# Optimization experiments

Measured on AMD Instinct MI355X. Metric: run time of the kernel, lower is better.

## Reference

```python
import jax, jax.numpy as jnp
import numpy as np

VOCAB_SIZE = 119547  # bert-base-multilingual-cased
B, S, H = 64, 512, 768


def setup_inputs() -> dict:
    key = jax.random.key(0)
    k1, k2, k3, k4 = jax.random.split(key, 4)
    hidden_states = jax.random.normal(k1, (B, S, H), dtype=jnp.float32)
    input_ids = jax.random.randint(k2, (B, S), 0, VOCAB_SIZE, dtype=jnp.int64)
    attention_mask = jnp.ones((B, S), dtype=jnp.int32)
    W1 = jax.random.normal(k3, (H, H), dtype=jnp.float32) * (1.0 / np.sqrt(H))
    b1 = jnp.zeros((H,), dtype=jnp.float32)
    W2 = jax.random.normal(k4, (H, 1), dtype=jnp.float32) * (1.0 / np.sqrt(H))
    b2 = jnp.zeros((1,), dtype=jnp.float32)
    return {"hidden_states": hidden_states, "input_ids": input_ids,
            "attention_mask": attention_mask, "W1": W1, "b1": b1, "W2": W2, "b2": b2}


def reference(hidden_states, input_ids, attention_mask, W1, b1, W2, b2):
    # token_importance MLP (dropout = identity at eval): [B,S,H] -> [B,S]
    h = jax.nn.relu(jnp.einsum('bsh,hk->bsk', hidden_states, W1) + b1)
    importance = (jnp.einsum('bsh,ho->bso', h, W2) + b2)[..., 0]  # [B,S]
    token_weights = jnp.log1p(jax.nn.relu(importance)) * attention_mask.astype(jnp.float32)
    # scatter-max into vocab-sized sparse doc vector.
    # Masked positions have weight 0; buffer init 0 and weights >= 0, so
    # scattering 0 is equivalent to skipping them (matches the torch loop).
    batch_idx = jnp.arange(hidden_states.shape[0])[:, None]  # [B,1]
    sparse_repr = jnp.zeros((hidden_states.shape[0], VOCAB_SIZE), dtype=token_weights.dtype)
    sparse_repr = sparse_repr.at[batch_idx, input_ids].max(token_weights)
    return sparse_repr, token_weights
```

## Files before the change

kernel.cpp:

```cpp
#include <hip/hip_runtime.h>
#include <math.h>
#include <stdint.h>

#define VOCAB 119547
#define NB    64
#define NS    512
#define NH    768
#define M_TOT (NB * NS)

typedef _Float16 half8_t __attribute__((ext_vector_type(8)));
typedef _Float16 half4_t __attribute__((ext_vector_type(4)));
typedef float f32x4 __attribute__((ext_vector_type(4)));

__device__ __forceinline__ void gload_lds16(const void* g, void* l) {
    __builtin_amdgcn_global_load_lds(
        (const __attribute__((address_space(1))) uint32_t*)g,
        (__attribute__((address_space(3))) uint32_t*)l, 16, 0, 0);
}

__global__ void prep(const float* __restrict__ W1,
                     float4* __restrict__ sparse4, float* __restrict__ imp_,
                     _Float16* __restrict__ W1T) {
    long i = (long)blockIdx.x * blockDim.x + threadIdx.x;
    long stride = (long)gridDim.x * blockDim.x;
    const float4 z = make_float4(0.f, 0.f, 0.f, 0.f);
    const long nsp4 = (long)NB * VOCAB / 4;
    for (long j = i; j < nsp4; j += stride) sparse4[j] = z;
    float4* imp4 = (float4*)imp_;
    for (long j = i; j < M_TOT / 4; j += stride) imp4[j] = z;
    const long nw4 = (long)NH * NH / 4;
    half4_t* W1T4 = (half4_t*)W1T;
    for (long j = i; j < nw4; j += stride) {
        int n  = (int)(j / (NH / 4));
        int k4 = (int)(j % (NH / 4)) * 4;
        half4_t h;
#pragma unroll
        for (int q = 0; q < 4; ++q) h[q] = (_Float16)W1[(long)(k4 + q) * NH + n];
        W1T4[j] = h;
    }
}

__global__ __launch_bounds__(256, 4) void gemm_f16(
    const float* __restrict__ X,
    const _Float16* __restrict__ W1T,
    const float* __restrict__ b1,
    const float* __restrict__ W2v,
    float* __restrict__ imp)
{
    __shared__ __align__(16) _Float16 As[2][128 * 32];
    __shared__ __align__(16) _Float16 Bs[2][128 * 32];

    const int tid  = threadIdx.x;
    const int lane = tid & 63;
    const int wid  = tid >> 6;
    const int wm   = wid >> 1;
    const int wn   = wid & 1;

    const int bid = blockIdx.x;
    const int wg  = (bid & 7) * 192 + (bid >> 3);
    const int nt  = wg % 6;
    const int mt  = wg / 6;
    const int m0  = mt * 128;
    const int n0  = nt * 128;

    const int c0 = tid, c1 = tid + 256;
    const int r0 = c0 >> 2, r1 = c1 >> 2;
    const int sk0 = ((c0 & 3) ^ ((r0 >> 1) & 3)) * 8;
    const int sk1 = ((c1 & 3) ^ ((r1 >> 1) & 3)) * 8;
    const _Float16* gB0 = W1T + (long)(n0 + r0) * NH + sk0;
    const _Float16* gB1 = W1T + (long)(n0 + r1) * NH + sk1;

    const int ar = tid >> 3;
    const int kc = tid & 7;
    const float* gA = X + (long)(m0 + ar) * NH + kc * 4;
    const int aw = ((kc >> 1) ^ ((ar >> 1) & 3)) * 8 + (kc & 1) * 4;

    const int lr = lane & 15;
    const int ls = lane >> 4;
    const int s2 = ls ^ ((lr >> 1) & 3);
    int offA[4], offB[4];
#pragma unroll
    for (int f = 0; f < 4; ++f) {
        offA[f] = (wm * 64 + f * 16 + lr) * 32 + s2 * 8;
        offB[f] = (wn * 64 + f * 16 + lr) * 32 + s2 * 8;
    }

    f32x4 acc[4][4];
#pragma unroll
    for (int a = 0; a < 4; ++a)
#pragma unroll
        for (int b = 0; b < 4; ++b) acc[a][b] = (f32x4){0.f, 0.f, 0.f, 0.f};

    float4 Areg[4];

#define LOADA(T)                                                            \
    _Pragma("unroll") for (int i = 0; i < 4; ++i)                           \
        Areg[i] = *(const float4*)(gA + (T) * 32 + (long)i * 32 * NH);

#define CVTWRITE(BUF)                                                       \
    _Pragma("unroll") for (int i = 0; i < 4; ++i) {                         \
        half4_t h;                                                          \
        h[0] = (_Float16)Areg[i].x; h[1] = (_Float16)Areg[i].y;             \
        h[2] = (_Float16)Areg[i].z; h[3] = (_Float16)Areg[i].w;             \
        *(half4_t*)(As[BUF] + (ar + 32 * i) * 32 + aw) = h;                 \
    }

#define STAGEB(T, BUF)                                                      \
    gload_lds16(gB0 + (T) * 32, Bs[BUF] + c0 * 8);                          \
    gload_lds16(gB1 + (T) * 32, Bs[BUF] + c1 * 8);

#define COMPUTE(BUF)                                                        \
    {                                                                       \
        half8_t af[4], bf[4];                                               \
        _Pragma("unroll") for (int f = 0; f < 4; ++f)                       \
            af[f] = *(const half8_t*)(As[BUF] + offA[f]);                   \
        _Pragma("unroll") for (int f = 0; f < 4; ++f)                       \
            bf[f] = *(const half8_t*)(Bs[BUF] + offB[f]);                   \
        _Pragma("unroll") for (int a = 0; a < 4; ++a)                       \
            _Pragma("unroll") for (int b = 0; b < 4; ++b)                   \
                acc[a][b] = __builtin_amdgcn_mfma_f32_16x16x32_f16(         \
                    af[a], bf[b], acc[a][b], 0, 0, 0);                      \
    }

#define KSTEP(T, CUR, NXT)                                                  \
    LOADA((T) + 1);                                                         \
    STAGEB((T) + 1, NXT);                                                   \
    COMPUTE(CUR);                                                           \
    CVTWRITE(NXT);                                                          \
    __syncthreads();

    LOADA(0);
    STAGEB(0, 0);
    CVTWRITE(0);
    __syncthreads();

#pragma unroll 1
    for (int t = 0; t < 22; t += 2) {
        KSTEP(t, 0, 1);
        KSTEP(t + 1, 1, 0);
    }
    KSTEP(22, 0, 1);
    COMPUTE(1);

#undef LOADA
#undef CVTWRITE
#undef STAGEB
#undef COMPUTE
#undef KSTEP

    float b1v[4], w2v[4];
#pragma unroll
    for (int f = 0; f < 4; ++f) {
        int col = n0 + wn * 64 + f * 16 + lr;
        b1v[f] = b1[col];
        w2v[f] = W2v[col];
    }
#pragma unroll
    for (int a = 0; a < 4; ++a)
#pragma unroll
        for (int reg = 0; reg < 4; ++reg) {
            float p = 0.f;
#pragma unroll
            for (int f = 0; f < 4; ++f) {
                float h = fmaxf(acc[a][f][reg] + b1v[f], 0.f);
                p = fmaf(h, w2v[f], p);
            }
            p += __shfl_xor(p, 1);
            p += __shfl_xor(p, 2);
            p += __shfl_xor(p, 4);
            p += __shfl_xor(p, 8);
            if (lr == 0) {
                int row = m0 + wm * 64 + a * 16 + ls * 4 + reg;
                atomicAdd(&imp[row], p);
            }
        }
}

__global__ void finalize(const float* __restrict__ imp,
                         const float* __restrict__ b2,
                         const int* __restrict__ mask,
                         const int* __restrict__ ids,
                         float* __restrict__ tw_out,
                         float* __restrict__ sparse) {
    int i = blockIdx.x * blockDim.x + threadIdx.x;
    if (i >= M_TOT) return;
    float v = fmaxf(imp[i] + b2[0], 0.f);
    float tw = log1pf(v) * (float)mask[i];
    tw_out[i] = tw;
    int b  = i >> 9;
    int id = ids[i];
    unsigned int* addr = (unsigned int*)&sparse[(long)b * VOCAB + id];
    atomicMax(addr, __float_as_uint(tw));
}

__global__ void zero_regions(float4* __restrict__ a, long na4,
                             float4* __restrict__ b, long nb4) {
    long i = (long)blockIdx.x * blockDim.x + threadIdx.x;
    long stride = (long)gridDim.x * blockDim.x;
    const float4 z = make_float4(0.f, 0.f, 0.f, 0.f);
    for (long j = i; j < na4; j += stride) a[j] = z;
    for (long j = i; j < nb4; j += stride) b[j] = z;
}

__global__ __launch_bounds__(256) void gemm_importance(
    const float* __restrict__ X, const float* __restrict__ W1,
    const float* __restrict__ b1, const float* __restrict__ W2v,
    float* __restrict__ imp)
{
    __shared__ float As_[16][64];
    __shared__ float Bs_[16][128];
    const int tid = threadIdx.x;
    const int m0 = blockIdx.x * 64, n0 = blockIdx.y * 128;
    const int tx = tid & 31, ty = tid >> 5;
    float acc[8][4];
#pragma unroll
    for (int r = 0; r < 8; ++r)
#pragma unroll
        for (int c = 0; c < 4; ++c) acc[r][c] = 0.f;
    const int arow = tid >> 2, ac = (tid & 3) * 4;
    const float* Xp = X + (long)(m0 + arow) * NH + ac;
    for (int k0 = 0; k0 < NH; k0 += 16) {
        float4 av = *(const float4*)(Xp + k0);
        As_[ac + 0][arow] = av.x; As_[ac + 1][arow] = av.y;
        As_[ac + 2][arow] = av.z; As_[ac + 3][arow] = av.w;
        int f = tid, br = f >> 5, bc = (f & 31) * 4;
        *(float4*)&Bs_[br][bc] = *(const float4*)&W1[(long)(k0 + br) * NH + n0 + bc];
        f = tid + 256; br = f >> 5; bc = (f & 31) * 4;
        *(float4*)&Bs_[br][bc] = *(const float4*)&W1[(long)(k0 + br) * NH + n0 + bc];
        __syncthreads();
#pragma unroll
        for (int k = 0; k < 16; ++k) {
            float4 a0 = *(const float4*)&As_[k][ty * 8];
            float4 a1 = *(const float4*)&As_[k][ty * 8 + 4];
            float4 bv = *(const float4*)&Bs_[k][tx * 4];
            float a[8] = {a0.x, a0.y, a0.z, a0.w, a1.x, a1.y, a1.z, a1.w};
            float bb[4] = {bv.x, bv.y, bv.z, bv.w};
#pragma unroll
            for (int r = 0; r < 8; ++r)
#pragma unroll
                for (int c = 0; c < 4; ++c)
                    acc[r][c] = fmaf(a[r], bb[c], acc[r][c]);
        }
        __syncthreads();
    }
    float b1v[4], w2v[4];
#pragma unroll
    for (int c = 0; c < 4; ++c) {
        int col = n0 + tx * 4 + c;
        b1v[c] = b1[col]; w2v[c] = W2v[col];
    }
#pragma unroll
    for (int r = 0; r < 8; ++r) {
        float p = 0.f;
#pragma unroll
        for (int c = 0; c < 4; ++c)
            p = fmaf(fmaxf(acc[r][c] + b1v[c], 0.f), w2v[c], p);
#pragma unroll
        for (int mdel = 16; mdel >= 1; mdel >>= 1) p += __shfl_xor(p, mdel);
        if (tx == 0) atomicAdd(&imp[m0 + ty * 8 + r], p);
    }
}

extern "C" void kernel_launch(void* const* d_in, const int* in_sizes, int n_in,
                              void* d_out, int out_size, void* d_ws, size_t ws_size,
                              hipStream_t stream) {
    const float* X    = (const float*)d_in[0];
    const int*   ids  = (const int*)d_in[1];
    const int*   mask = (const int*)d_in[2];
    const float* W1   = (const float*)d_in[3];
    const float* b1   = (const float*)d_in[4];
    const float* W2   = (const float*)d_in[5];
    const float* b2   = (const float*)d_in[6];

    float* sparse = (float*)d_out;
    float* tw_out = sparse + (long)NB * VOCAB;
    float* imp    = (float*)d_ws;

    const size_t impB = (size_t)M_TOT * 4;
    const size_t W1TB = (size_t)NH * NH * 2;
    const size_t need = impB + W1TB;

    if (ws_size >= need) {
        _Float16* W1T = (_Float16*)((char*)d_ws + impB);
        prep<<<1024, 256, 0, stream>>>(W1, (float4*)sparse, imp, W1T);
        gemm_f16<<<(M_TOT / 128) * (NH / 128), 256, 0, stream>>>(
            X, W1T, b1, W2, imp);
        finalize<<<M_TOT / 256, 256, 0, stream>>>(imp, b2, mask, ids, tw_out, sparse);
    } else {
        zero_regions<<<2048, 256, 0, stream>>>(
            (float4*)sparse, (long)NB * VOCAB / 4, (float4*)imp, M_TOT / 4);
        dim3 grid(M_TOT / 64, NH / 128);
        gemm_importance<<<grid, 256, 0, stream>>>(X, W1, b1, W2, imp);
        finalize<<<M_TOT / 256, 256, 0, stream>>>(imp, b2, mask, ids, tw_out, sparse);
    }
}
```

Baseline: 249.1 us.

## Deepen A-tile register prefetch with manual waitcnts and use memset for zeroing

The GEMM main loop now double-buffers the fp32 A-tile register loads, issuing loads two k-steps ahead. It replaces __syncthreads with explicit vmcnt/lgkmcnt waits, raw s_barrier and sched_barrier fences, so global latency can overlap more compute. Zeroing of the sparse output and the importance buffer moves from a grid-stride kernel to hipMemsetAsync, and W1 transposition becomes its own small kernel. The hand-counted waitcnt values risk ordering bugs if the compiler emits a different number of memory ops, and the extra A registers may affect occupancy.

```diff
diff --git a/kernel.cpp b/kernel.cpp
--- a/kernel.cpp
+++ b/kernel.cpp
@@ -12,32 +12,25 @@
 typedef _Float16 half4_t __attribute__((ext_vector_type(4)));
 typedef float f32x4 __attribute__((ext_vector_type(4)));
 
+#define WAITVM(N) asm volatile("s_waitcnt vmcnt(" #N ")" ::: "memory")
+#define WAITLGKM() asm volatile("s_waitcnt lgkmcnt(0)" ::: "memory")
+#define SCHEDB() __builtin_amdgcn_sched_barrier(0)
+
 __device__ __forceinline__ void gload_lds16(const void* g, void* l) {
     __builtin_amdgcn_global_load_lds(
         (const __attribute__((address_space(1))) uint32_t*)g,
         (__attribute__((address_space(3))) uint32_t*)l, 16, 0, 0);
 }
 
-__global__ void prep(const float* __restrict__ W1,
-                     float4* __restrict__ sparse4, float* __restrict__ imp_,
-                     _Float16* __restrict__ W1T) {
+__global__ void prep_w1t(const float* __restrict__ W1, _Float16* __restrict__ W1T) {
     long i = (long)blockIdx.x * blockDim.x + threadIdx.x;
-    long stride = (long)gridDim.x * blockDim.x;
-    const float4 z = make_float4(0.f, 0.f, 0.f, 0.f);
-    const long nsp4 = (long)NB * VOCAB / 4;
-    for (long j = i; j < nsp4; j += stride) sparse4[j] = z;
-    float4* imp4 = (float4*)imp_;
-    for (long j = i; j < M_TOT / 4; j += stride) imp4[j] = z;
-    const long nw4 = (long)NH * NH / 4;
-    half4_t* W1T4 = (half4_t*)W1T;
-    for (long j = i; j < nw4; j += stride) {
-        int n  = (int)(j / (NH / 4));
-        int k4 = (int)(j % (NH / 4)) * 4;
-        half4_t h;
-#pragma unroll
-        for (int q = 0; q < 4; ++q) h[q] = (_Float16)W1[(long)(k4 + q) * NH + n];
-        W1T4[j] = h;
-    }
+    if (i >= (long)NH * NH / 4) return;
+    int n  = (int)(i / (NH / 4));
+    int k4 = (int)(i % (NH / 4)) * 4;
+    half4_t h;
+#pragma unroll
+    for (int q = 0; q < 4; ++q) h[q] = (_Float16)W1[(long)(k4 + q) * NH + n];
+    ((half4_t*)W1T)[i] = h;
 }
 
 __global__ __launch_bounds__(256, 4) void gemm_f16(
@@ -91,17 +84,17 @@
 #pragma unroll
         for (int b = 0; b < 4; ++b) acc[a][b] = (f32x4){0.f, 0.f, 0.f, 0.f};
 
-    float4 Areg[4];
-
-#define LOADA(T)                                                            \
+    float4 ArA[4], ArB[4];
+
+#define LOADA(T, AR)                                                        \
     _Pragma("unroll") for (int i = 0; i < 4; ++i)                           \
-        Areg[i] = *(const float4*)(gA + (T) * 32 + (long)i * 32 * NH);
-
-#define CVTWRITE(BUF)                                                       \
+        AR[i] = *(const float4*)(gA + (T) * 32 + (long)i * 32 * NH);
+
+#define CVTWRITE(BUF, AR)                                                   \
     _Pragma("unroll") for (int i = 0; i < 4; ++i) {                         \
         half4_t h;                                                          \
-        h[0] = (_Float16)Areg[i].x; h[1] = (_Float16)Areg[i].y;             \
-        h[2] = (_Float16)Areg[i].z; h[3] = (_Float16)Areg[i].w;             \
+        h[0] = (_Float16)AR[i].x; h[1] = (_Float16)AR[i].y;                 \
+        h[2] = (_Float16)AR[i].z; h[3] = (_Float16)AR[i].w;                 \
         *(half4_t*)(As[BUF] + (ar + 32 * i) * 32 + aw) = h;                 \
     }
 
@@ -122,24 +115,35 @@
                     af[a], bf[b], acc[a][b], 0, 0, 0);                      \
     }
 
-#define KSTEP(T, CUR, NXT)                                                  \
-    LOADA((T) + 1);                                                         \
+#define KSTEP(T, CUR, NXT, ARC, ARL)                                        \
     STAGEB((T) + 1, NXT);                                                   \
+    SCHEDB();                                                               \
+    LOADA(((T) + 2 > 23 ? 23 : (T) + 2), ARL);                              \
     COMPUTE(CUR);                                                           \
-    CVTWRITE(NXT);                                                          \
-    __syncthreads();
-
-    LOADA(0);
+    WAITVM(6);                                                              \
+    CVTWRITE(NXT, ARC);                                                     \
+    WAITVM(4);                                                              \
+    WAITLGKM();                                                             \
+    __builtin_amdgcn_s_barrier();                                           \
+    SCHEDB();
+
+    LOADA(0, ArA);
+    SCHEDB();
     STAGEB(0, 0);
-    CVTWRITE(0);
-    __syncthreads();
+    WAITVM(2);
+    CVTWRITE(0, ArA);
+    LOADA(1, ArA);
+    WAITVM(4);
+    WAITLGKM();
+    __builtin_amdgcn_s_barrier();
+    SCHEDB();
 
 #pragma unroll 1
     for (int t = 0; t < 22; t += 2) {
-        KSTEP(t, 0, 1);
-        KSTEP(t + 1, 1, 0);
-    }
-    KSTEP(22, 0, 1);
+        KSTEP(t, 0, 1, ArA, ArB);
+        KSTEP(t + 1, 1, 0, ArB, ArA);
+    }
+    KSTEP(22, 0, 1, ArA, ArB);
     COMPUTE(1);
 
 #undef LOADA
@@ -193,15 +197,6 @@
     atomicMax(addr, __float_as_uint(tw));
 }
 
-__global__ void zero_regions(float4* __restrict__ a, long na4,
-                             float4* __restrict__ b, long nb4) {
-    long i = (long)blockIdx.x * blockDim.x + threadIdx.x;
-    long stride = (long)gridDim.x * blockDim.x;
-    const float4 z = make_float4(0.f, 0.f, 0.f, 0.f);
-    for (long j = i; j < na4; j += stride) a[j] = z;
-    for (long j = i; j < nb4; j += stride) b[j] = z;
-}
-
 __global__ __launch_bounds__(256) void gemm_importance(
     const float* __restrict__ X, const float* __restrict__ W1,
     const float* __restrict__ b1, const float* __restrict__ W2v,
@@ -278,19 +273,18 @@
 
     const size_t impB = (size_t)M_TOT * 4;
     const size_t W1TB = (size_t)NH * NH * 2;
-    const size_t need = impB + W1TB;
-
-    if (ws_size >= need) {
+
+    hipMemsetAsync(sparse, 0, (size_t)NB * VOCAB * 4, stream);
+    hipMemsetAsync(imp, 0, impB, stream);
+
+    if (ws_size >= impB + W1TB) {
         _Float16* W1T = (_Float16*)((char*)d_ws + impB);
-        prep<<<1024, 256, 0, stream>>>(W1, (float4*)sparse, imp, W1T);
+        prep_w1t<<<(NH * NH / 4 + 255) / 256, 256, 0, stream>>>(W1, W1T);
         gemm_f16<<<(M_TOT / 128) * (NH / 128), 256, 0, stream>>>(
             X, W1T, b1, W2, imp);
-        finalize<<<M_TOT / 256, 256, 0, stream>>>(imp, b2, mask, ids, tw_out, sparse);
     } else {
-        zero_regions<<<2048, 256, 0, stream>>>(
-            (float4*)sparse, (long)NB * VOCAB / 4, (float4*)imp, M_TOT / 4);
         dim3 grid(M_TOT / 64, NH / 128);
         gemm_importance<<<grid, 256, 0, stream>>>(X, W1, b1, W2, imp);
-        finalize<<<M_TOT / 256, 256, 0, stream>>>(imp, b2, mask, ids, tw_out, sparse);
-    }
-}
+    }
+    finalize<<<M_TOT / 256, 256, 0, stream>>>(imp, b2, mask, ids, tw_out, sparse);
+}
```

Result: slower. 266.0 us (+6.8%).
